# Optimization experiments

Hardware: AMD Instinct MI355X
Metric: run time of the kernel (lower is better)

The kernel has to match this reference:

```python
import jax, jax.numpy as jnp
import numpy as np

SCALES = (2, 4, 8)  # primitive_scales, one per branch


def setup_inputs() -> dict:
    key = jax.random.key(0)
    k0, k1, k2, k3, k4 = jax.random.split(key, 5)
    B, C, H, W = 16, 256, 128, 128
    s = 1.0 / np.sqrt(C).astype(np.float32)
    return {
        "x": jax.random.normal(k0, (B, C, H, W), jnp.float32),
        "W_proto": jax.random.normal(k1, (3, C, C), jnp.float32) * s,
        "W_frame": jax.random.normal(k2, (3, C, C), jnp.float32) * s,
        "W_out": jax.random.normal(k3, (3, C, C), jnp.float32) * s,
        "W_fuse": jax.random.normal(k4, (C, 3 * C), jnp.float32) * (1.0 / np.sqrt(3 * C).astype(np.float32)),
    }


def _branch(x, Wp, Wf, Wo, P):
    # x: [B,C,H,W]; adaptive_avg_pool2d(x, (H, P)) with W % P == 0 == mean over equal bins along W
    B, C, H, W = x.shape
    proto = x.reshape(B, C, H, P, W // P).mean(axis=-1)        # [B,C,H,P]
    proto = jnp.einsum('oc,bchp->bohp', Wp, proto)             # proto_proj (1x1 conv)
    q = jnp.einsum('oc,bchw->bhwo', Wf, x)                     # frame_proj + permute -> [B,H,W,C]
    # att = q @ k, k = proto.permute(0,2,1,3) -> [B,H,C,P]
    att = jnp.einsum('bhwc,bchp->bhwp', q, proto) * (1.0 / jnp.sqrt(jnp.float32(C)))
    att = jax.nn.softmax(att, axis=-1)                         # [B,H,W,P]
    # v = proto.permute(0,2,3,1) -> [B,H,P,C]; msg = att @ v -> [B,H,W,C]
    msg = jnp.einsum('bhwp,bchp->bhwc', att, proto)
    return jnp.einsum('oc,bhwc->bohw', Wo, msg)                # out_proj -> [B,C,H,W]


def reference(x, W_proto, W_frame, W_out, W_fuse):
    outs = [_branch(x, W_proto[i], W_frame[i], W_out[i], SCALES[i]) for i in range(len(SCALES))]
    cat = jnp.concatenate(outs, axis=1)                        # [B, 3C, H, W]
    return jnp.einsum('oc,bchw->bohw', W_fuse, cat) + x
```

## Files before the change

kernel.cpp:

```cpp
#include <hip/hip_runtime.h>
#include <hip/hip_bf16.h>
#include <math.h>

#define CC   256
#define HW   (128*128)
#define MAT  (CC*CC)
#define NBH  2048
#define N0   4096
#define N1   8192
#define N2   16384

typedef __attribute__((ext_vector_type(8))) short bf16x8;
typedef __attribute__((ext_vector_type(4))) float f32x4;

__global__ __launch_bounds__(256) void k_mats1(
    const float* __restrict__ Wp, const float* __restrict__ Wf,
    const float* __restrict__ Wo, const float* __restrict__ Wfu,
    __hip_bfloat16* __restrict__ A, float* __restrict__ E)
{
    int idx = blockIdx.x;
    int t = threadIdx.x;
    if (idx < 3*CC) {
        int i = idx >> 8, c = idx & 255;
        const float* wf = Wf + (size_t)i*MAT;
        const float* wp = Wp + (size_t)i*MAT;
        float acc = 0.f;
        for (int o = 0; o < CC; ++o)
            acc += wf[o*CC + c] * wp[o*CC + t];
        A[(size_t)i*512*CC + (size_t)c*CC + t] = __float2bfloat16(acc);
    } else {
        idx -= 3*CC;
        int i = idx >> 8, o = idx & 255;
        const float* wo = Wo + (size_t)i*MAT;
        const float* wfu = Wfu + (size_t)o*(3*CC) + i*CC;
        float acc = 0.f;
        for (int c3 = 0; c3 < CC; ++c3)
            acc += wfu[c3] * wo[c3*CC + t];
        E[(size_t)i*MAT + (size_t)o*CC + t] = acc;
    }
}

__global__ __launch_bounds__(256) void k_mats2(
    const float* __restrict__ Wp, const float* __restrict__ E,
    __hip_bfloat16* __restrict__ A)
{
    int idx = blockIdx.x;
    int i = idx >> 8, o = idx & 255;
    int t = threadIdx.x;
    const float* e = E + (size_t)i*MAT + (size_t)o*CC;
    const float* wp = Wp + (size_t)i*MAT;
    float acc = 0.f;
    for (int c = 0; c < CC; ++c)
        acc += e[c] * wp[c*CC + t];
    A[(size_t)i*512*CC + (size_t)(256+o)*CC + t] = __float2bfloat16(acc);
}

__global__ __launch_bounds__(256) void k_pool(
    const float* __restrict__ x, __hip_bfloat16* __restrict__ Bt)
{
    int t = threadIdx.x;
    int hh = t >> 7;
    int cg = (t >> 5) & 3;
    int q  = t & 31;
    int bh = blockIdx.x*2 + hh;
    int b = bh >> 7, h = bh & 127;
    __shared__ float bins[2][256][9];
    size_t rowbase = ((size_t)b*CC)*HW + (size_t)h*128;
    #pragma unroll 4
    for (int cc = 0; cc < 64; ++cc) {
        int c = cc*4 + cg;
        float4 v = *reinterpret_cast<const float4*>(&x[rowbase + (size_t)c*HW + q*4]);
        float s = v.x + v.y + v.z + v.w;
        s += __shfl_xor(s, 1);
        s += __shfl_xor(s, 2);
        if ((q & 3) == 0) bins[hh][c][q >> 2] = s;
    }
    __syncthreads();
    __hip_bfloat16* B0 = Bt;
    __hip_bfloat16* B1 = Bt + (size_t)N0*CC;
    __hip_bfloat16* B2 = Bt + (size_t)(N0+N1)*CC;
    #pragma unroll 2
    for (int rep = 0; rep < 2; ++rep) {
        int c = rep*128 + (t & 127);
        int hh2 = t >> 7;
        int bh2 = blockIdx.x*2 + hh2;
        float b8[8];
        #pragma unroll
        for (int j = 0; j < 8; ++j) b8[j] = bins[hh2][c][j];
        B0[((size_t)bh2*2 + 0)*CC + c] = __float2bfloat16((b8[0]+b8[1]+b8[2]+b8[3]) * (1.f/64.f));
        B0[((size_t)bh2*2 + 1)*CC + c] = __float2bfloat16((b8[4]+b8[5]+b8[6]+b8[7]) * (1.f/64.f));
        #pragma unroll
        for (int j = 0; j < 4; ++j)
            B1[((size_t)bh2*4 + j)*CC + c] = __float2bfloat16((b8[2*j]+b8[2*j+1]) * (1.f/32.f));
        #pragma unroll
        for (int j = 0; j < 8; ++j)
            B2[((size_t)bh2*8 + j)*CC + c] = __float2bfloat16(b8[j] * (1.f/16.f));
    }
}

__global__ __launch_bounds__(128) void k_gemm(
    const __hip_bfloat16* __restrict__ A,
    const __hip_bfloat16* __restrict__ Bt,
    float* __restrict__ Cc)
{
    int blk = blockIdx.x;
    int br, lb, LP, poff;
    if (blk < 256)      { br = 0; lb = blk;       LP = 1; poff = 0; }
    else if (blk < 768) { br = 1; lb = blk - 256; LP = 2; poff = 2; }
    else                { br = 2; lb = blk - 768; LP = 3; poff = 6; }
    size_t aoff  = (size_t)br*512*CC;
    size_t btoff = (br == 0) ? 0 : (br == 1 ? (size_t)N0*CC : (size_t)(N0+N1)*CC);
    const __hip_bfloat16* Ab = A  + aoff;
    const __hip_bfloat16* Bb = Bt + btoff;

    int rb = lb & 3, cb = lb >> 2;
    int wv = threadIdx.x >> 6, lane = threadIdx.x & 63;
    int row0 = rb*128 + wv*64;
    int col0 = cb*64;
    int lr = lane & 15, lk = (lane >> 4) * 8;

    f32x4 acc[4][4] = {};
    for (int kk = 0; kk < CC; kk += 32) {
        bf16x8 af[4], bfr[4];
        #pragma unroll
        for (int m = 0; m < 4; ++m)
            af[m] = *reinterpret_cast<const bf16x8*>(Ab + (size_t)(row0 + m*16 + lr)*CC + kk + lk);
        #pragma unroll
        for (int n = 0; n < 4; ++n)
            bfr[n] = *reinterpret_cast<const bf16x8*>(Bb + (size_t)(col0 + n*16 + lr)*CC + kk + lk);
        #pragma unroll
        for (int m = 0; m < 4; ++m)
            #pragma unroll
            for (int n = 0; n < 4; ++n)
                acc[m][n] = __builtin_amdgcn_mfma_f32_16x16x32_bf16(af[m], bfr[n], acc[m][n], 0, 0, 0);
    }

    int cr = (lane >> 4) * 4, ccol = lane & 15;
    int pm = (1 << LP) - 1;
    #pragma unroll
    for (int m = 0; m < 4; ++m) {
        #pragma unroll
        for (int n = 0; n < 4; ++n) {
            int colg = col0 + n*16 + ccol;
            int bh = colg >> LP, p = colg & pm;
            float* dst = Cc + (size_t)bh*8192 + poff + p;
            #pragma unroll
            for (int j = 0; j < 4; ++j) {
                int r = row0 + m*16 + cr + j;
                dst[r*16] = acc[m][n][j];
            }
        }
    }
}

template<int L>
__device__ __forceinline__ void softmax_l(float* a) {
    float m = a[0];
    #pragma unroll
    for (int j = 1; j < L; ++j) m = fmaxf(m, a[j]);
    float s = 0.f;
    #pragma unroll
    for (int j = 0; j < L; ++j) { a[j] = __expf(a[j] - m); s += a[j]; }
    float r = 1.f / s;
    #pragma unroll
    for (int j = 0; j < L; ++j) a[j] *= r;
}

__global__ __launch_bounds__(256) void k_main(
    const float* __restrict__ x, const float* __restrict__ Cc,
    float* __restrict__ out)
{
    int bh = blockIdx.x;
    int b = bh >> 7, h = bh & 127;
    int t = threadIdx.x;
    int w = t & 127;
    int g = __builtin_amdgcn_readfirstlane(t >> 7);
    const float* Cb = Cc + (size_t)bh * 8192;
    size_t base = ((size_t)b*CC)*HW + (size_t)h*128 + w;
    __shared__ float att_s[128][17];

    float att[14];
    #pragma unroll
    for (int p = 0; p < 14; ++p) att[p] = 0.f;

    #pragma unroll 4
    for (int cc = 0; cc < 128; ++cc) {
        int c = cc*2 + g;
        float xv = x[base + (size_t)c*HW];
        const float* mp = Cb + c*16;
        #pragma unroll
        for (int p = 0; p < 14; ++p) att[p] += xv * mp[p];
    }

    if (g == 1) {
        #pragma unroll
        for (int p = 0; p < 14; ++p) att_s[w][p] = att[p];
    }
    __syncthreads();
    if (g == 0) {
        #pragma unroll
        for (int p = 0; p < 14; ++p) att[p] = (att[p] + att_s[w][p]) * 0.0625f;
        softmax_l<2>(att + 0);
        softmax_l<4>(att + 2);
        softmax_l<8>(att + 6);
        #pragma unroll
        for (int p = 0; p < 14; ++p) att_s[w][p] = att[p];
    }
    __syncthreads();
    #pragma unroll
    for (int p = 0; p < 14; ++p) att[p] = att_s[w][p];

    #pragma unroll 2
    for (int oo = 0; oo < 128; ++oo) {
        int o = oo*2 + g;
        float acc = x[base + (size_t)o*HW];
        const float* vp = Cb + (256 + o)*16;
        #pragma unroll
        for (int p = 0; p < 14; ++p) acc += att[p] * vp[p];
        out[base + (size_t)o*HW] = acc;
    }
}

extern "C" void kernel_launch(void* const* d_in, const int* in_sizes, int n_in,
                              void* d_out, int out_size, void* d_ws, size_t ws_size,
                              hipStream_t stream)
{
    (void)in_sizes; (void)n_in; (void)out_size; (void)ws_size;
    const float* x   = (const float*)d_in[0];
    const float* Wp  = (const float*)d_in[1];
    const float* Wf  = (const float*)d_in[2];
    const float* Wo  = (const float*)d_in[3];
    const float* Wfu = (const float*)d_in[4];
    float* out = (float*)d_out;

    char* wsb = (char*)d_ws;
    float*          E  = (float*)wsb;
    __hip_bfloat16* A  = (__hip_bfloat16*)(wsb + 786432);
    __hip_bfloat16* Bt = (__hip_bfloat16*)(wsb + 1572864);
    float*          Cc = (float*)(wsb + 16252928);

    k_mats1<<<dim3(6*CC),  dim3(256), 0, stream>>>(Wp, Wf, Wo, Wfu, A, E);
    k_mats2<<<dim3(3*CC),  dim3(256), 0, stream>>>(Wp, E, A);
    k_pool <<<dim3(NBH/2), dim3(256), 0, stream>>>(x, Bt);
    k_gemm <<<dim3(1792),  dim3(128), 0, stream>>>(A, Bt, Cc);
    k_main <<<dim3(NBH),   dim3(256), 0, stream>>>(x, Cc, out);
}
```

Before: 395.4 us.

## Split pooling into contiguous per-channel reduction and regroup pass; widen main kernel loads

Pooling now runs in two kernels. The first reads each (b,c) plane contiguously and writes fp32 bin sums to a workspace that aliases the Cc buffer. The second transposes those sums into the bf16 per-scale matrices, replacing the old strided per-row reads. The main kernel now has each thread handle two adjacent pixels with float2 loads and stores, and splits channels across four waves instead of two, with a shared-memory reduction. The goal is better coalescing and more memory-level parallelism, at the cost of an extra launch, an intermediate round trip through global memory, and higher register use.

```diff
diff --git a/kernel.cpp b/kernel.cpp
--- a/kernel.cpp
+++ b/kernel.cpp
@@ -55,47 +55,53 @@
     A[(size_t)i*512*CC + (size_t)(256+o)*CC + t] = __float2bfloat16(acc);
 }
 
-__global__ __launch_bounds__(256) void k_pool(
-    const float* __restrict__ x, __hip_bfloat16* __restrict__ Bt)
-{
-    int t = threadIdx.x;
-    int hh = t >> 7;
-    int cg = (t >> 5) & 3;
-    int q  = t & 31;
-    int bh = blockIdx.x*2 + hh;
-    int b = bh >> 7, h = bh & 127;
-    __shared__ float bins[2][256][9];
-    size_t rowbase = ((size_t)b*CC)*HW + (size_t)h*128;
+__global__ __launch_bounds__(256) void k_poolA(
+    const float* __restrict__ x, float* __restrict__ binsG)
+{
+    int bc = blockIdx.x;
+    int t = threadIdx.x;
+    const float4* xp = (const float4*)(x + (size_t)bc*HW);
+    __shared__ float bins[128][9];
+    int hb = t >> 5;
+    int bin = (t & 31) >> 2;
     #pragma unroll 4
-    for (int cc = 0; cc < 64; ++cc) {
-        int c = cc*4 + cg;
-        float4 v = *reinterpret_cast<const float4*>(&x[rowbase + (size_t)c*HW + q*4]);
+    for (int i = 0; i < 16; ++i) {
+        float4 v = xp[i*256 + t];
         float s = v.x + v.y + v.z + v.w;
         s += __shfl_xor(s, 1);
         s += __shfl_xor(s, 2);
-        if ((q & 3) == 0) bins[hh][c][q >> 2] = s;
+        if ((t & 3) == 0) bins[i*8 + hb][bin] = s;
     }
     __syncthreads();
+    int h = t >> 1, b0 = (t & 1) * 4;
+    float4 o;
+    o.x = bins[h][b0+0]; o.y = bins[h][b0+1];
+    o.z = bins[h][b0+2]; o.w = bins[h][b0+3];
+    ((float4*)binsG)[(size_t)bc*256 + t] = o;
+}
+
+__global__ __launch_bounds__(256) void k_poolB(
+    const float* __restrict__ binsG, __hip_bfloat16* __restrict__ Bt)
+{
+    int bh = blockIdx.x;
+    int b = bh >> 7, h = bh & 127;
+    int c = threadIdx.x;
+    const float* g = binsG + (((size_t)b*256 + c)*128 + h)*8;
+    float4 lo = *(const float4*)(g);
+    float4 hi = *(const float4*)(g + 4);
+    float b8[8] = {lo.x, lo.y, lo.z, lo.w, hi.x, hi.y, hi.z, hi.w};
+
     __hip_bfloat16* B0 = Bt;
     __hip_bfloat16* B1 = Bt + (size_t)N0*CC;
     __hip_bfloat16* B2 = Bt + (size_t)(N0+N1)*CC;
-    #pragma unroll 2
-    for (int rep = 0; rep < 2; ++rep) {
-        int c = rep*128 + (t & 127);
-        int hh2 = t >> 7;
-        int bh2 = blockIdx.x*2 + hh2;
-        float b8[8];
-        #pragma unroll
-        for (int j = 0; j < 8; ++j) b8[j] = bins[hh2][c][j];
-        B0[((size_t)bh2*2 + 0)*CC + c] = __float2bfloat16((b8[0]+b8[1]+b8[2]+b8[3]) * (1.f/64.f));
-        B0[((size_t)bh2*2 + 1)*CC + c] = __float2bfloat16((b8[4]+b8[5]+b8[6]+b8[7]) * (1.f/64.f));
-        #pragma unroll
-        for (int j = 0; j < 4; ++j)
-            B1[((size_t)bh2*4 + j)*CC + c] = __float2bfloat16((b8[2*j]+b8[2*j+1]) * (1.f/32.f));
-        #pragma unroll
-        for (int j = 0; j < 8; ++j)
-            B2[((size_t)bh2*8 + j)*CC + c] = __float2bfloat16(b8[j] * (1.f/16.f));
-    }
+    B0[((size_t)bh*2 + 0)*CC + c] = __float2bfloat16((b8[0]+b8[1]+b8[2]+b8[3]) * (1.f/64.f));
+    B0[((size_t)bh*2 + 1)*CC + c] = __float2bfloat16((b8[4]+b8[5]+b8[6]+b8[7]) * (1.f/64.f));
+    #pragma unroll
+    for (int j = 0; j < 4; ++j)
+        B1[((size_t)bh*4 + j)*CC + c] = __float2bfloat16((b8[2*j]+b8[2*j+1]) * (1.f/32.f));
+    #pragma unroll
+    for (int j = 0; j < 8; ++j)
+        B2[((size_t)bh*8 + j)*CC + c] = __float2bfloat16(b8[j] * (1.f/16.f));
 }
 
 __global__ __launch_bounds__(128) void k_gemm(
@@ -154,16 +160,19 @@
 }
 
 template<int L>
-__device__ __forceinline__ void softmax_l(float* a) {
-    float m = a[0];
-    #pragma unroll
-    for (int j = 1; j < L; ++j) m = fmaxf(m, a[j]);
-    float s = 0.f;
-    #pragma unroll
-    for (int j = 0; j < L; ++j) { a[j] = __expf(a[j] - m); s += a[j]; }
-    float r = 1.f / s;
-    #pragma unroll
-    for (int j = 0; j < L; ++j) a[j] *= r;
+__device__ __forceinline__ void softmax2(float2* a) {
+    float mx = a[0].x, my = a[0].y;
+    #pragma unroll
+    for (int j = 1; j < L; ++j) { mx = fmaxf(mx, a[j].x); my = fmaxf(my, a[j].y); }
+    float sx = 0.f, sy = 0.f;
+    #pragma unroll
+    for (int j = 0; j < L; ++j) {
+        a[j].x = __expf(a[j].x - mx); sx += a[j].x;
+        a[j].y = __expf(a[j].y - my); sy += a[j].y;
+    }
+    float rx = 1.f / sx, ry = 1.f / sy;
+    #pragma unroll
+    for (int j = 0; j < L; ++j) { a[j].x *= rx; a[j].y *= ry; }
 }
 
 __global__ __launch_bounds__(256) void k_main(
@@ -173,51 +182,62 @@
     int bh = blockIdx.x;
     int b = bh >> 7, h = bh & 127;
     int t = threadIdx.x;
-    int w = t & 127;
-    int g = __builtin_amdgcn_readfirstlane(t >> 7);
+    int lane = t & 63;
+    int wv = __builtin_amdgcn_readfirstlane(t >> 6);
     const float* Cb = Cc + (size_t)bh * 8192;
-    size_t base = ((size_t)b*CC)*HW + (size_t)h*128 + w;
-    __shared__ float att_s[128][17];
-
-    float att[14];
-    #pragma unroll
-    for (int p = 0; p < 14; ++p) att[p] = 0.f;
-
-    #pragma unroll 4
-    for (int cc = 0; cc < 128; ++cc) {
-        int c = cc*2 + g;
-        float xv = x[base + (size_t)c*HW];
+    size_t base2 = (((size_t)b*CC)*HW + (size_t)h*128) >> 1;
+    const float2* x2 = (const float2*)x;
+    float2* out2 = (float2*)out;
+    __shared__ float2 att_s[4][64][14];
+
+    float2 att[14];
+    #pragma unroll
+    for (int p = 0; p < 14; ++p) att[p] = make_float2(0.f, 0.f);
+
+    #pragma unroll 8
+    for (int cc = 0; cc < 64; ++cc) {
+        int c = cc*4 + wv;
+        float2 xv = x2[base2 + (size_t)c*(HW/2) + lane];
         const float* mp = Cb + c*16;
         #pragma unroll
-        for (int p = 0; p < 14; ++p) att[p] += xv * mp[p];
-    }
-
-    if (g == 1) {
-        #pragma unroll
-        for (int p = 0; p < 14; ++p) att_s[w][p] = att[p];
-    }
+        for (int p = 0; p < 14; ++p) {
+            att[p].x += xv.x * mp[p];
+            att[p].y += xv.y * mp[p];
+        }
+    }
+
+    #pragma unroll
+    for (int p = 0; p < 14; ++p) att_s[wv][lane][p] = att[p];
     __syncthreads();
-    if (g == 0) {
-        #pragma unroll
-        for (int p = 0; p < 14; ++p) att[p] = (att[p] + att_s[w][p]) * 0.0625f;
-        softmax_l<2>(att + 0);
-        softmax_l<4>(att + 2);
-        softmax_l<8>(att + 6);
-        #pragma unroll
-        for (int p = 0; p < 14; ++p) att_s[w][p] = att[p];
+    if (wv == 0) {
+        #pragma unroll
+        for (int p = 0; p < 14; ++p) {
+            float2 a1 = att_s[1][lane][p], a2 = att_s[2][lane][p], a3 = att_s[3][lane][p];
+            att[p].x = (att[p].x + a1.x + a2.x + a3.x) * 0.0625f;
+            att[p].y = (att[p].y + a1.y + a2.y + a3.y) * 0.0625f;
+        }
+        softmax2<2>(att + 0);
+        softmax2<4>(att + 2);
+        softmax2<8>(att + 6);
+        #pragma unroll
+        for (int p = 0; p < 14; ++p) att_s[0][lane][p] = att[p];
     }
     __syncthreads();
     #pragma unroll
-    for (int p = 0; p < 14; ++p) att[p] = att_s[w][p];
-
-    #pragma unroll 2
-    for (int oo = 0; oo < 128; ++oo) {
-        int o = oo*2 + g;
-        float acc = x[base + (size_t)o*HW];
+    for (int p = 0; p < 14; ++p) att[p] = att_s[0][lane][p];
+
+    #pragma unroll 8
+    for (int oo = 0; oo < 64; ++oo) {
+        int o = oo*4 + wv;
+        float2 xv = x2[base2 + (size_t)o*(HW/2) + lane];
         const float* vp = Cb + (256 + o)*16;
-        #pragma unroll
-        for (int p = 0; p < 14; ++p) acc += att[p] * vp[p];
-        out[base + (size_t)o*HW] = acc;
+        float2 acc = xv;
+        #pragma unroll
+        for (int p = 0; p < 14; ++p) {
+            acc.x += att[p].x * vp[p];
+            acc.y += att[p].y * vp[p];
+        }
+        out2[base2 + (size_t)o*(HW/2) + lane] = acc;
     }
 }
 
@@ -234,14 +254,16 @@
     float* out = (float*)d_out;
 
     char* wsb = (char*)d_ws;
-    float*          E  = (float*)wsb;
-    __hip_bfloat16* A  = (__hip_bfloat16*)(wsb + 786432);
-    __hip_bfloat16* Bt = (__hip_bfloat16*)(wsb + 1572864);
-    float*          Cc = (float*)(wsb + 16252928);
+    float*          E     = (float*)wsb;
+    __hip_bfloat16* A     = (__hip_bfloat16*)(wsb + 786432);
+    __hip_bfloat16* Bt    = (__hip_bfloat16*)(wsb + 1572864);
+    float*          Cc    = (float*)(wsb + 16252928);
+    float*          binsG = Cc;
 
     k_mats1<<<dim3(6*CC),  dim3(256), 0, stream>>>(Wp, Wf, Wo, Wfu, A, E);
     k_mats2<<<dim3(3*CC),  dim3(256), 0, stream>>>(Wp, E, A);
-    k_pool <<<dim3(NBH/2), dim3(256), 0, stream>>>(x, Bt);
+    k_poolA<<<dim3(4096),  dim3(256), 0, stream>>>(x, binsG);
+    k_poolB<<<dim3(NBH),   dim3(256), 0, stream>>>(binsG, Bt);
     k_gemm <<<dim3(1792),  dim3(128), 0, stream>>>(A, Bt, Cc);
     k_main <<<dim3(NBH),   dim3(256), 0, stream>>>(x, Cc, out);
 }
```

Result: faster. 342.3 us (-13.5%).
